# Kernel tuning notes

Measured on AMD Instinct MI355X. Metric: run time of the kernel, lower is better.

Reference implementation:

```python
import jax, jax.numpy as jnp
import numpy as np

B, N0, NCLS = 8, 1024, 40
SPACING, SIGMA_FACTOR = 2.0, 1.0
BLOCKS = [[64, 64], [128, 128], [256, 1024]]
POOL_SIZES = [256, 64, 1]
FC1, FC2 = 512, 256
# 3x3x3 kernel translation grid (27-point support, hard-coded in ConvLayer)
GRID = jnp.asarray(np.array([[i, j, k] for i in (-1, 0, 1) for j in (-1, 0, 1) for k in (-1, 0, 1)], dtype=np.float32))  # [27,3]


def pcnn_conv(pc, feat, W, b, sigma):
    """Extension-operator point convolution.
    pc [B,N,3], feat [B,N,Cin], W [27,Cin,Cout], b [Cout].
    out[b,i,o] = relu( (1/N) * sum_l sum_j exp(-||p_i - p_j + t_l||^2/(2 ks^2)) f[b,j] @ W[l] + b )
    """
    ks = SIGMA_FACTOR * sigma
    trans = SPACING * sigma * GRID                      # [27,3]
    inv = 1.0 / (2.0 * ks * ks)
    diff = pc[:, :, None, :] - pc[:, None, :, :]        # [B,N,N,3]
    d2 = jnp.sum(diff * diff, -1)                       # [B,N,N]
    n = pc.shape[1]

    def body(acc, wt):
        t, Wl = wt                                      # t [3], Wl [Cin,Cout]
        # ||diff + t||^2 = d2 + 2 diff.t + |t|^2
        e = jnp.exp(-(d2 + 2.0 * jnp.einsum('bijd,d->bij', diff, t) + jnp.dot(t, t)) * inv)
        s = jnp.einsum('bij,bjc->bic', e, feat)         # Gaussian-weighted gather
        return acc + jnp.einsum('bic,co->bio', s, Wl), None

    out0 = jnp.zeros((pc.shape[0], n, W.shape[2]), feat.dtype)
    out, _ = jax.lax.scan(body, out0, (trans, W))
    return jax.nn.relu(out / n + b)


def fps(pts, m):
    """Farthest point sampling. pts [N,3] -> indices [m]."""
    d = jnp.sum((pts - pts[0]) ** 2, -1)
    idxs = jnp.zeros((m,), jnp.int32)

    def body(i, state):
        idxs, d = state
        nxt = jnp.argmax(d).astype(jnp.int32)
        idxs = idxs.at[i].set(nxt)
        d = jnp.minimum(d, jnp.sum((pts - pts[nxt]) ** 2, -1))
        return idxs, d

    idxs, _ = jax.lax.fori_loop(1, m, body, (idxs, d))
    return idxs


def pool(pc, feat, m):
    """FPS subsample to m centers, max-pool features over nearest-center clusters."""
    idx = jax.vmap(lambda p: fps(p, m))(pc)                      # [B,m]
    centers = jnp.take_along_axis(pc, idx[..., None], axis=1)    # [B,m,3]
    dist = jnp.sum((pc[:, :, None, :] - centers[:, None, :, :]) ** 2, -1)  # [B,N,m]
    assign = jnp.argmin(dist, -1)                                # [B,N]
    pooled = jax.vmap(lambda f, a: jax.ops.segment_max(f, a, num_segments=m))(feat, assign)
    return centers, pooled


def bn(x, g, b):
    mu = jnp.mean(x, 0)
    v = jnp.var(x, 0)
    return g * (x - mu) * jax.lax.rsqrt(v + 1e-5) + b


def setup_inputs() -> dict:
    key = jax.random.key(0)
    ks = jax.random.split(key, 24)
    inp = {"pc": jax.random.normal(ks[0], (B, 3, N0), jnp.float32)}
    chans = [4, 64, 64, 128, 128, 256, 1024]
    for i, (ci, co) in enumerate(zip(chans[:-1], chans[1:])):
        inp[f"w_c{i}"] = jax.random.normal(ks[1 + i], (27, ci, co), jnp.float32) * 0.05
        inp[f"b_c{i}"] = jnp.zeros((co,), jnp.float32)
    inp["w_fc1"] = jax.random.normal(ks[10], (1024, FC1), jnp.float32) * 0.03
    inp["g_fc1"] = jnp.ones((FC1,), jnp.float32)
    inp["be_fc1"] = jnp.zeros((FC1,), jnp.float32)
    inp["w_fc2"] = jax.random.normal(ks[11], (FC1, FC2), jnp.float32) * 0.05
    inp["g_fc2"] = jnp.ones((FC2,), jnp.float32)
    inp["be_fc2"] = jnp.zeros((FC2,), jnp.float32)
    inp["w_fc3"] = jax.random.normal(ks[12], (FC2, NCLS), jnp.float32) * 0.05
    inp["b_fc3"] = jnp.zeros((NCLS,), jnp.float32)
    return inp


def reference(pc, w_c0, b_c0, w_c1, b_c1, w_c2, b_c2, w_c3, b_c3, w_c4, b_c4, w_c5, b_c5,
              w_fc1, g_fc1, be_fc1, w_fc2, g_fc2, be_fc2, w_fc3, b_fc3):
    pts = jnp.transpose(pc, (0, 2, 1))                           # [B,N,3]
    b_, n0, _ = pts.shape
    feat = jnp.concatenate([pts, jnp.ones((b_, n0, 1), pts.dtype)], -1)  # [B,N,4]
    sigma = 1.0 / float(np.sqrt(n0))  # faithfully uses initial N for all blocks
    ws = [(w_c0, b_c0), (w_c1, b_c1), (w_c2, b_c2), (w_c3, b_c3), (w_c4, b_c4), (w_c5, b_c5)]
    idx = 0
    cur = pts
    for bi, block in enumerate(BLOCKS):
        for _ in block:
            W, bb = ws[idx]
            feat = pcnn_conv(cur, feat, W, bb, sigma)
            idx += 1
        cur, feat = pool(cur, feat, POOL_SIZES[bi])
    x = feat.reshape(b_, -1)                                     # [B,1024]
    x = jax.nn.relu(bn(x @ w_fc1, g_fc1, be_fc1))
    x = jax.nn.relu(bn(x @ w_fc2, g_fc2, be_fc2))
    return x @ w_fc3 + b_fc3
```

## Files before the change

kernel.cpp:

```cpp
#include <hip/hip_runtime.h>
#include <cstdint>
#include <cstddef>
#include <cmath>

constexpr int B = 8;
constexpr int N0 = 1024;
constexpr int CAP = 64;
using u16 = unsigned short;

typedef __bf16 bf16x8 __attribute__((ext_vector_type(8)));
typedef float f32x4 __attribute__((ext_vector_type(4)));

__device__ inline u16 f2bf(float x) {
  unsigned u = __float_as_uint(x);
  return (u16)((u + 0x7fffu + ((u >> 16) & 1u)) >> 16);
}
__device__ inline float bf2f(u16 h) { return __uint_as_float(((unsigned)h) << 16); }
__device__ inline int swk2(int row, int k) {
  int s = (((row >> 2) ^ (row >> 4)) & 3);
  return ((((k >> 3) ^ s) << 3) | (k & 7));
}

__global__ __launch_bounds__(256) void k_prep(const float* __restrict__ pc,
                                              float* __restrict__ pts,
                                              float* __restrict__ feat0,
                                              uint4* __restrict__ p3, int n3,
                                              uint4* __restrict__ p6, int n6,
                                              uint4* __restrict__ p9, int n9) {
  int idx = blockIdx.x * blockDim.x + threadIdx.x;
  if (idx < B * N0) {
    int b = idx / N0, i = idx - b * N0;
    float x = pc[(b * 3 + 0) * N0 + i];
    float y = pc[(b * 3 + 1) * N0 + i];
    float z = pc[(b * 3 + 2) * N0 + i];
    pts[idx * 3 + 0] = x; pts[idx * 3 + 1] = y; pts[idx * 3 + 2] = z;
    feat0[idx * 4 + 0] = x; feat0[idx * 4 + 1] = y; feat0[idx * 4 + 2] = z; feat0[idx * 4 + 3] = 1.0f;
  }
  uint4 v = make_uint4(0xFFFFFFFFu, 0xFFFFFFFFu, 0xFFFFFFFFu, 0xFFFFFFFFu);
  for (int i = idx; i < n3; i += B * N0) p3[i] = v;
  for (int i = idx; i < n6; i += B * N0) p6[i] = v;
  for (int i = idx; i < n9; i += B * N0) p9[i] = v;
}

__global__ __launch_bounds__(256) void k_pairs(const float* __restrict__ pts,
                                               int* __restrict__ pidx, int* __restrict__ pcnt,
                                               int N) {
  const int r = blockIdx.x * 4 + (threadIdx.x >> 6);
  const int lane = threadIdx.x & 63;
  const int b = r / N;
  const float px = pts[(size_t)r * 3 + 0];
  const float py = pts[(size_t)r * 3 + 1];
  const float pz = pts[(size_t)r * 3 + 2];
  int* row = pidx + (size_t)r * CAP;
  int base = 0;
  for (int j0 = 0; j0 < N; j0 += 64) {
    int j = j0 + lane;
    float dx = px - pts[((size_t)b * N + j) * 3 + 0];
    float dy = py - pts[((size_t)b * N + j) * 3 + 1];
    float dz = pz - pts[((size_t)b * N + j) * 3 + 2];
    float d2 = dx * dx + dy * dy + dz * dz;
    bool keep = d2 <= 0.1228f;
    unsigned long long mk = __ballot(keep);
    int pos = __popcll(mk & ((1ull << lane) - 1ull));
    if (keep) { int s = base + pos; if (s < CAP) row[s] = j; }
    base += __popcll(mk);
  }
  if (lane == 0) pcnt[r] = base < CAP ? base : CAP;
}

__global__ void k_econtract(const float* __restrict__ pts, const float* __restrict__ feat,
                            const int* __restrict__ pidx, const int* __restrict__ pcnt,
                            u16* __restrict__ Shi, u16* __restrict__ Slo,
                            int N, int Cin, int K, int Kpad, int mbase) {
  const int g = mbase + blockIdx.x;
  const int b = g / N;
  const int t = threadIdx.x;
  const bool cact = t < Cin;
  const float px = pts[(size_t)g * 3 + 0];
  const float py = pts[(size_t)g * 3 + 1];
  const float pz = pts[(size_t)g * 3 + 2];
  float acc[27];
#pragma unroll
  for (int l = 0; l < 27; ++l) acc[l] = 0.f;
  const int n = pcnt[g];
  const int* row = pidx + (size_t)g * CAP;
  for (int p = 0; p < n; ++p) {
    int j = row[p];
    size_t jb = (size_t)b * N + j;
    float dx = px - pts[jb * 3 + 0];
    float dy = py - pts[jb * 3 + 1];
    float dz = pz - pts[jb * 3 + 2];
    float d2 = dx * dx + dy * dy + dz * dz;
    float base_ = __expf(-512.f * d2);
    float gxv[3] = {__expf(64.f * dx - 2.f), 1.f, __expf(-64.f * dx - 2.f)};
    float gyv[3] = {__expf(64.f * dy - 2.f), 1.f, __expf(-64.f * dy - 2.f)};
    float gzv[3] = {__expf(64.f * dz - 2.f), 1.f, __expf(-64.f * dz - 2.f)};
    float fv = cact ? feat[jb * Cin + t] : 0.f;
#pragma unroll
    for (int a = 0; a < 3; ++a) {
      float ba = base_ * gxv[a];
#pragma unroll
      for (int b2 = 0; b2 < 3; ++b2) {
        float bab = ba * gyv[b2];
#pragma unroll
        for (int c2 = 0; c2 < 3; ++c2) {
          int l = a * 9 + b2 * 3 + c2;
          acc[l] = fmaf(bab * gzv[c2], fv, acc[l]);
        }
      }
    }
  }
  size_t rowo = (size_t)blockIdx.x * Kpad;
  if (cact) {
#pragma unroll
    for (int l = 0; l < 27; ++l) {
      float v = acc[l];
      u16 h = f2bf(v);
      u16 lo = f2bf(v - bf2f(h));
      Shi[rowo + (size_t)l * Cin + t] = h;
      Slo[rowo + (size_t)l * Cin + t] = lo;
    }
  }
  if (Kpad > K && t >= Cin && t < Cin + (Kpad - K)) {
    size_t po = rowo + K + (t - Cin);
    Shi[po] = 0; Slo[po] = 0;
  }
}

__global__ __launch_bounds__(512) void k_gemm_mfma(const u16* __restrict__ Shi,
                                                   const u16* __restrict__ Slo,
                                                   const float* __restrict__ W,
                                                   const float* __restrict__ bias,
                                                   float* __restrict__ out,
                                                   float* __restrict__ P,
                                                   int K, int Kpad, int Cout, float scale,
                                                   int mcur) {
  __shared__ u16 As[2][2][32][40];
  __shared__ u16 Bs[2][2][64][40];
  __shared__ float xch[4][64][8];
  const int t = threadIdx.x;
  const int h = t >> 8;
  const int tl = t & 255;
  const int nb = blockIdx.x * 64;
  const int m0 = blockIdx.y * 32;
  const int l = t & 63, w = t >> 6;
  const int ks = w >> 2, wq = w & 3;
  const int wm = (wq >> 1) * 16, wn = (wq & 1) * 32;
  const int la = l & 15, lg = l >> 4;
  const int ntiles = Kpad >> 6;
  const int KZ = gridDim.z, z = blockIdx.z;
  const int q = ntiles / KZ, r = ntiles % KZ;
  const int t0 = z * q + (z < r ? z : r);
  const int cnt = q + (z < r ? 1 : 0);
  const int ar = tl >> 3, ak = (tl & 7) * 4;
  const size_t aOff = (size_t)(m0 + ar) * Kpad + h * 32 + ak;
  const int aw = swk2(ar, ak);
  const int kp = (tl >> 4) * 2, n4 = (tl & 15) * 4;
  f32x4 acc0 = {0.f, 0.f, 0.f, 0.f}, acc1 = {0.f, 0.f, 0.f, 0.f};

  for (int kt = 0; kt < cnt; ++kt) {
    const int k0 = (t0 + kt) * 64;
    *(ushort4*)&As[h][0][ar][aw] = *(const ushort4*)(Shi + aOff + k0);
    *(ushort4*)&As[h][1][ar][aw] = *(const ushort4*)(Slo + aOff + k0);
    {
      int gk0 = k0 + h * 32 + kp;
      float4 b0 = make_float4(0.f, 0.f, 0.f, 0.f), b1 = b0;
      if (gk0 < K) b0 = *(const float4*)(W + (size_t)gk0 * Cout + nb + n4);
      if (gk0 + 1 < K) b1 = *(const float4*)(W + (size_t)(gk0 + 1) * Cout + nb + n4);
      float v0[4] = {b0.x, b0.y, b0.z, b0.w};
      float v1[4] = {b1.x, b1.y, b1.z, b1.w};
#pragma unroll
      for (int e = 0; e < 4; ++e) {
        int n = n4 + e;
        int kw = swk2(n, kp);
        u16 h0 = f2bf(v0[e]);
        u16 l0 = f2bf(v0[e] - bf2f(h0));
        u16 h1 = f2bf(v1[e]);
        u16 l1 = f2bf(v1[e] - bf2f(h1));
        *(unsigned*)&Bs[h][0][n][kw] = (unsigned)h0 | ((unsigned)h1 << 16);
        *(unsigned*)&Bs[h][1][n][kw] = (unsigned)l0 | ((unsigned)l1 << 16);
      }
    }
    __syncthreads();
    bf16x8 ah = *(const bf16x8*)&As[ks][0][wm + la][swk2(wm + la, lg * 8)];
    bf16x8 al = *(const bf16x8*)&As[ks][1][wm + la][swk2(wm + la, lg * 8)];
    bf16x8 bh0 = *(const bf16x8*)&Bs[ks][0][wn + la][swk2(wn + la, lg * 8)];
    bf16x8 bl0 = *(const bf16x8*)&Bs[ks][1][wn + la][swk2(wn + la, lg * 8)];
    bf16x8 bh1 = *(const bf16x8*)&Bs[ks][0][wn + 16 + la][swk2(wn + 16 + la, lg * 8)];
    bf16x8 bl1 = *(const bf16x8*)&Bs[ks][1][wn + 16 + la][swk2(wn + 16 + la, lg * 8)];
    acc0 = __builtin_amdgcn_mfma_f32_16x16x32_bf16(ah, bh0, acc0, 0, 0, 0);
    acc1 = __builtin_amdgcn_mfma_f32_16x16x32_bf16(ah, bh1, acc1, 0, 0, 0);
    acc0 = __builtin_amdgcn_mfma_f32_16x16x32_bf16(al, bh0, acc0, 0, 0, 0);
    acc1 = __builtin_amdgcn_mfma_f32_16x16x32_bf16(al, bh1, acc1, 0, 0, 0);
    acc0 = __builtin_amdgcn_mfma_f32_16x16x32_bf16(ah, bl0, acc0, 0, 0, 0);
    acc1 = __builtin_amdgcn_mfma_f32_16x16x32_bf16(ah, bl1, acc1, 0, 0, 0);
    __syncthreads();
  }
  if (w >= 4) {
#pragma unroll
    for (int r2 = 0; r2 < 4; ++r2) { xch[wq][l][r2] = acc0[r2]; xch[wq][l][r2 + 4] = acc1[r2]; }
  }
  __syncthreads();
  if (w < 4) {
#pragma unroll
    for (int r2 = 0; r2 < 4; ++r2) { acc0[r2] += xch[wq][l][r2]; acc1[r2] += xch[wq][l][r2 + 4]; }
    if (gridDim.z == 1) {
#pragma unroll
      for (int r2 = 0; r2 < 4; ++r2) {
        int gm = m0 + wm + lg * 4 + r2;
        int gn0 = nb + wn + la;
        out[(size_t)gm * Cout + gn0] = fmaxf(fmaf(acc0[r2], scale, bias[gn0]), 0.f);
        int gn1 = gn0 + 16;
        out[(size_t)gm * Cout + gn1] = fmaxf(fmaf(acc1[r2], scale, bias[gn1]), 0.f);
      }
    } else {
      float* Pz = P + (size_t)z * mcur * Cout;
#pragma unroll
      for (int r2 = 0; r2 < 4; ++r2) {
        int gm = m0 + wm + lg * 4 + r2;
        int gn0 = nb + wn + la;
        Pz[(size_t)gm * Cout + gn0] = acc0[r2];
        Pz[(size_t)gm * Cout + gn0 + 16] = acc1[r2];
      }
    }
  }
}

__global__ __launch_bounds__(256) void k_reduce(const float* __restrict__ P,
                                                const float* __restrict__ bias,
                                                float* __restrict__ out,
                                                int n4, int Cout, int KZ, float scale,
                                                int stride) {
  int i = blockIdx.x * 256 + threadIdx.x;
  if (i >= n4) return;
  float4 s = *(const float4*)(P + (size_t)i * 4);
  for (int z = 1; z < KZ; ++z) {
    float4 v = *(const float4*)(P + (size_t)z * stride + (size_t)i * 4);
    s.x += v.x; s.y += v.y; s.z += v.z; s.w += v.w;
  }
  int c = (i * 4) % Cout;
  float4 bb = *(const float4*)(bias + c);
  float4 o;
  o.x = fmaxf(fmaf(s.x, scale, bb.x), 0.f);
  o.y = fmaxf(fmaf(s.y, scale, bb.y), 0.f);
  o.z = fmaxf(fmaf(s.z, scale, bb.z), 0.f);
  o.w = fmaxf(fmaf(s.w, scale, bb.w), 0.f);
  *(float4*)(out + (size_t)i * 4) = o;
}

template <int CTRL>
__device__ __forceinline__ float dppmaxf(float v) {
  int o = __builtin_amdgcn_update_dpp(0, __float_as_int(v), CTRL, 0xF, 0xF, true);
  return fmaxf(v, __int_as_float(o));
}
__device__ __forceinline__ float wavemaxf(float v) {
  v = dppmaxf<0xB1>(v);
  v = dppmaxf<0x4E>(v);
  v = dppmaxf<0x141>(v);
  v = dppmaxf<0x140>(v);
  v = dppmaxf<0x142>(v);
  v = dppmaxf<0x143>(v);
  return __uint_as_float((unsigned)__builtin_amdgcn_readlane(__float_as_int(v), 63));
}

#define FPS_LOAD(i) \
  float qx##i = src[3 * i + 0], qy##i = src[3 * i + 1], qz##i = src[3 * i + 2];
#define FPS_PIN(i) \
  asm volatile("" : "+v"(qx##i), "+v"(qy##i), "+v"(qz##i));
#define FPS_D0(i) \
  float d##i; { float ax = __fsub_rn(qx##i, x0), ay = __fsub_rn(qy##i, y0), az = __fsub_rn(qz##i, z0); \
    d##i = __fadd_rn(__fadd_rn(__fmul_rn(ax, ax), __fmul_rn(ay, ay)), __fmul_rn(az, az)); }
#define FPS_UPD(i) \
  { float ax = __fsub_rn(qx##i, cx), ay = __fsub_rn(qy##i, cy), az = __fsub_rn(qz##i, cz); \
    float nd = __fadd_rn(__fadd_rn(__fmul_rn(ax, ax), __fmul_rn(ay, ay)), __fmul_rn(az, az)); \
    d##i = fminf(d##i, nd); }
#define FPS_SEL(i) \
  { bool e = (d##i == lbest); sx = e ? qx##i : sx; sy = e ? qy##i : sy; sz = e ? qz##i : sz; }

__global__ __launch_bounds__(64, 1) void k_fps1024(const float* __restrict__ pts,
                                                   float* __restrict__ centers, int m) {
  const int b = blockIdx.x;
  const int t = threadIdx.x;
  const float* P = pts + (size_t)b * 1024 * 3;
  const float* src = P + t * 16 * 3;
  FPS_LOAD(0) FPS_LOAD(1) FPS_LOAD(2) FPS_LOAD(3)
  FPS_LOAD(4) FPS_LOAD(5) FPS_LOAD(6) FPS_LOAD(7)
  FPS_LOAD(8) FPS_LOAD(9) FPS_LOAD(10) FPS_LOAD(11)
  FPS_LOAD(12) FPS_LOAD(13) FPS_LOAD(14) FPS_LOAD(15)
  FPS_PIN(0) FPS_PIN(1) FPS_PIN(2) FPS_PIN(3)
  FPS_PIN(4) FPS_PIN(5) FPS_PIN(6) FPS_PIN(7)
  FPS_PIN(8) FPS_PIN(9) FPS_PIN(10) FPS_PIN(11)
  FPS_PIN(12) FPS_PIN(13) FPS_PIN(14) FPS_PIN(15)
  float x0 = P[0], y0 = P[1], z0 = P[2];
  FPS_D0(0) FPS_D0(1) FPS_D0(2) FPS_D0(3)
  FPS_D0(4) FPS_D0(5) FPS_D0(6) FPS_D0(7)
  FPS_D0(8) FPS_D0(9) FPS_D0(10) FPS_D0(11)
  FPS_D0(12) FPS_D0(13) FPS_D0(14) FPS_D0(15)
  if (t == 0) {
    centers[(size_t)b * m * 3 + 0] = x0;
    centers[(size_t)b * m * 3 + 1] = y0;
    centers[(size_t)b * m * 3 + 2] = z0;
  }
  for (int it = 1; it < m; ++it) {
    float lbest;
    {
      float a0 = fmaxf(d0, d1), a1 = fmaxf(d2, d3), a2 = fmaxf(d4, d5), a3 = fmaxf(d6, d7);
      float a4 = fmaxf(d8, d9), a5 = fmaxf(d10, d11), a6 = fmaxf(d12, d13), a7 = fmaxf(d14, d15);
      float b0 = fmaxf(a0, a1), b1 = fmaxf(a2, a3), b2 = fmaxf(a4, a5), b3 = fmaxf(a6, a7);
      lbest = fmaxf(fmaxf(b0, b1), fmaxf(b2, b3));
    }
    float sx = qx15, sy = qy15, sz = qz15;
    FPS_SEL(14) FPS_SEL(13) FPS_SEL(12) FPS_SEL(11)
    FPS_SEL(10) FPS_SEL(9) FPS_SEL(8) FPS_SEL(7)
    FPS_SEL(6) FPS_SEL(5) FPS_SEL(4) FPS_SEL(3)
    FPS_SEL(2) FPS_SEL(1) FPS_SEL(0)
    float wmax = wavemaxf(lbest);
    unsigned long long mask = __ballot(lbest == wmax);
    int fl = __ffsll((long long)mask) - 1;
    float cx = __uint_as_float((unsigned)__builtin_amdgcn_readlane(__float_as_int(sx), fl));
    float cy = __uint_as_float((unsigned)__builtin_amdgcn_readlane(__float_as_int(sy), fl));
    float cz = __uint_as_float((unsigned)__builtin_amdgcn_readlane(__float_as_int(sz), fl));
    if (t == 0) {
      centers[((size_t)b * m + it) * 3 + 0] = cx;
      centers[((size_t)b * m + it) * 3 + 1] = cy;
      centers[((size_t)b * m + it) * 3 + 2] = cz;
    }
    FPS_UPD(0) FPS_UPD(1) FPS_UPD(2) FPS_UPD(3)
    FPS_UPD(4) FPS_UPD(5) FPS_UPD(6) FPS_UPD(7)
    FPS_UPD(8) FPS_UPD(9) FPS_UPD(10) FPS_UPD(11)
    FPS_UPD(12) FPS_UPD(13) FPS_UPD(14) FPS_UPD(15)
  }
}

__global__ __launch_bounds__(64, 1) void k_fps256(const float* __restrict__ pts,
                                                  float* __restrict__ centers, int m) {
  const int b = blockIdx.x;
  const int t = threadIdx.x;
  const float* P = pts + (size_t)b * 256 * 3;
  const float* src = P + t * 4 * 3;
  FPS_LOAD(0) FPS_LOAD(1) FPS_LOAD(2) FPS_LOAD(3)
  FPS_PIN(0) FPS_PIN(1) FPS_PIN(2) FPS_PIN(3)
  float x0 = P[0], y0 = P[1], z0 = P[2];
  FPS_D0(0) FPS_D0(1) FPS_D0(2) FPS_D0(3)
  if (t == 0) {
    centers[(size_t)b * m * 3 + 0] = x0;
    centers[(size_t)b * m * 3 + 1] = y0;
    centers[(size_t)b * m * 3 + 2] = z0;
  }
  for (int it = 1; it < m; ++it) {
    float lbest = fmaxf(fmaxf(d0, d1), fmaxf(d2, d3));
    float sx = qx3, sy = qy3, sz = qz3;
    FPS_SEL(2) FPS_SEL(1) FPS_SEL(0)
    float wmax = wavemaxf(lbest);
    unsigned long long mask = __ballot(lbest == wmax);
    int fl = __ffsll((long long)mask) - 1;
    float cx = __uint_as_float((unsigned)__builtin_amdgcn_readlane(__float_as_int(sx), fl));
    float cy = __uint_as_float((unsigned)__builtin_amdgcn_readlane(__float_as_int(sy), fl));
    float cz = __uint_as_float((unsigned)__builtin_amdgcn_readlane(__float_as_int(sz), fl));
    if (t == 0) {
      centers[((size_t)b * m + it) * 3 + 0] = cx;
      centers[((size_t)b * m + it) * 3 + 1] = cy;
      centers[((size_t)b * m + it) * 3 + 2] = cz;
    }
    FPS_UPD(0) FPS_UPD(1) FPS_UPD(2) FPS_UPD(3)
  }
}

__global__ __launch_bounds__(64) void k_center0(const float* __restrict__ pts,
                                                float* __restrict__ centers,
                                                int* __restrict__ assign) {
  const int b = blockIdx.x, t = threadIdx.x;
  if (t < 3) centers[b * 3 + t] = pts[(size_t)b * 64 * 3 + t];
  assign[b * 64 + t] = 0;
}

__global__ __launch_bounds__(256) void k_assign(const float* __restrict__ pts,
                                                const float* __restrict__ centers,
                                                int* __restrict__ assign, int N, int m) {
  __shared__ float cs[256 * 3];
  const int t = threadIdx.x;
  const int idx = blockIdx.x * 256 + t;
  const int b = (blockIdx.x * 256) / N;
  for (int i = t; i < m * 3; i += 256) cs[i] = centers[(size_t)b * m * 3 + i];
  __syncthreads();
  float px = pts[(size_t)idx * 3 + 0], py = pts[(size_t)idx * 3 + 1], pz = pts[(size_t)idx * 3 + 2];
  float best = 3.4e38f; int bk = 0;
  for (int k = 0; k < m; ++k) {
    float dx = __fsub_rn(px, cs[k * 3 + 0]);
    float dy = __fsub_rn(py, cs[k * 3 + 1]);
    float dz = __fsub_rn(pz, cs[k * 3 + 2]);
    float dd = __fadd_rn(__fadd_rn(__fmul_rn(dx, dx), __fmul_rn(dy, dy)), __fmul_rn(dz, dz));
    if (dd < best) { best = dd; bk = k; }
  }
  assign[idx] = bk;
}

__global__ __launch_bounds__(256) void k_segmax(const float* __restrict__ feat,
                                                const int* __restrict__ assign,
                                                float* __restrict__ pooled,
                                                int N, int m, int C) {
  int idx = blockIdx.x * blockDim.x + threadIdx.x;
  if (idx >= B * N * C) return;
  int b = idx / (N * C);
  int r = idx - b * N * C;
  int i = r / C;
  int c = r - i * C;
  int a = assign[b * N + i];
  atomicMax((int*)&pooled[((size_t)b * m + a) * C + c], __float_as_int(feat[idx]));
}

template <int K, int COUT, bool BNR>
__global__ __launch_bounds__(256) void k_fc(const float* __restrict__ x,
                                            const float* __restrict__ w,
                                            const float* __restrict__ g,
                                            const float* __restrict__ be,
                                            float* __restrict__ out) {
  __shared__ float ys[8][33];
  int t = threadIdx.x;
  int n = t >> 5, cl = t & 31;
  int c = blockIdx.x * 32 + cl;
  float acc = 0.f;
  if (c < COUT) {
    const float* xr = x + n * K;
    float a0 = 0.f, a1 = 0.f, a2 = 0.f, a3 = 0.f;
    for (int k = 0; k < K; k += 4) {
      a0 = fmaf(xr[k + 0], w[(size_t)(k + 0) * COUT + c], a0);
      a1 = fmaf(xr[k + 1], w[(size_t)(k + 1) * COUT + c], a1);
      a2 = fmaf(xr[k + 2], w[(size_t)(k + 2) * COUT + c], a2);
      a3 = fmaf(xr[k + 3], w[(size_t)(k + 3) * COUT + c], a3);
    }
    acc = (a0 + a1) + (a2 + a3);
  }
  ys[n][cl] = acc;
  __syncthreads();
  if (c >= COUT) return;
  if (BNR) {
    float mu = 0.f;
#pragma unroll
    for (int q = 0; q < 8; ++q) mu += ys[q][cl];
    mu *= 0.125f;
    float var = 0.f;
#pragma unroll
    for (int q = 0; q < 8; ++q) { float dv = ys[q][cl] - mu; var = fmaf(dv, dv, var); }
    var *= 0.125f;
    float rs = 1.f / sqrtf(var + 1e-5f);
    float v = g[c] * (acc - mu) * rs + be[c];
    out[n * COUT + c] = fmaxf(v, 0.f);
  } else {
    out[n * COUT + c] = acc + be[c];
  }
}

extern "C" void kernel_launch(void* const* d_in, const int* in_sizes, int n_in,
                              void* d_out, int out_size, void* d_ws, size_t ws_size,
                              hipStream_t stream) {
  (void)in_sizes; (void)n_in; (void)out_size;
  const float* pc = (const float*)d_in[0];
  const float* Wc[6]; const float* bc[6];
  for (int l = 0; l < 6; ++l) { Wc[l] = (const float*)d_in[1 + 2 * l]; bc[l] = (const float*)d_in[2 + 2 * l]; }
  const float* w1 = (const float*)d_in[13];
  const float* g1 = (const float*)d_in[14];
  const float* be1 = (const float*)d_in[15];
  const float* w2 = (const float*)d_in[16];
  const float* g2 = (const float*)d_in[17];
  const float* be2 = (const float*)d_in[18];
  const float* w3 = (const float*)d_in[19];
  const float* b3 = (const float*)d_in[20];

  float* ws = (float*)d_ws;
  size_t o = 0;
  auto A = [&](size_t n) { size_t r = o; o += (n + 63) & ~(size_t)63; return r; };
  const size_t PTS0 = A((size_t)B * 1024 * 3);
  const size_t PTS1 = A((size_t)B * 256 * 3);
  const size_t PTS2 = A((size_t)B * 64 * 3);
  const size_t PTS3 = A((size_t)B * 3);
  const size_t F0  = A((size_t)B * 1024 * 4);
  const size_t FB1 = A((size_t)B * 1024 * 64);
  const size_t FB2 = A((size_t)B * 1024 * 64);
  const size_t FB3 = A((size_t)B * 256 * 64);
  const size_t FB4 = A((size_t)B * 256 * 128);
  const size_t FB5 = A((size_t)B * 256 * 128);
  const size_t FB6 = A((size_t)B * 64 * 128);
  const size_t FB7 = A((size_t)B * 64 * 256);
  const size_t FB8 = A((size_t)B * 64 * 1024);
  const size_t FB9 = A((size_t)B * 1024);
  const size_t ASSIGN = A((size_t)B * 1024);
  const size_t Y1 = A((size_t)8 * 512);
  const size_t Y2 = A((size_t)8 * 256);
  const size_t PIDX = A((size_t)B * 1024 * CAP);
  const size_t PCNT = A((size_t)B * 1024);
  const size_t dynB = o * sizeof(float);

  int* pidx = (int*)(ws + PIDX);
  int* pcnt = (int*)(ws + PCNT);

  k_prep<<<dim3((B * N0 + 255) / 256), dim3(256), 0, stream>>>(
      pc, ws + PTS0, ws + F0,
      (uint4*)(ws + FB3), B * 256 * 64 / 4,
      (uint4*)(ws + FB6), B * 64 * 128 / 4,
      (uint4*)(ws + FB9), B * 1024 / 4);

  auto conv = [&](size_t ptsOff, size_t finOff, size_t foutOff, int Npts, int Cin, int Cout,
                  const float* W, const float* bias) {
    const int M = B * Npts;
    const int K = 27 * Cin;
    const int Kpad = (K + 63) & ~63;
    const size_t availB = (ws_size > dynB) ? ws_size - dynB : 0;
    size_t pResB = availB / 4;
    if (pResB > (size_t)13 << 20) pResB = (size_t)13 << 20;
    const size_t sByte = availB - pResB;
    long mc = (long)(sByte / ((size_t)Kpad * 4)) & ~31L;
    int Mc = (int)((mc < (long)M) ? mc : (long)M);
    if (Mc < 32) Mc = 32;
    u16* Shi = (u16*)((char*)d_ws + dynB);
    u16* Slo = Shi + (size_t)Mc * Kpad;
    float* P = (float*)(Shi + (size_t)2 * Mc * Kpad);
    const int mch = (M + Mc - 1) / Mc;
    const float scale = 1.f / (float)Npts;
    const int blk = (Cin <= 64) ? 64 : Cin;
    const int ntiles = Kpad >> 6;
    for (int mcb = 0; mcb < mch; ++mcb) {
      const int mb0 = mcb * Mc;
      const int mcur = ((M - mb0) < Mc) ? (M - mb0) : Mc;
      k_econtract<<<dim3(mcur), dim3(blk), 0, stream>>>(ws + ptsOff, ws + finOff, pidx, pcnt,
                                                        Shi, Slo, Npts, Cin, K, Kpad, mb0);
      const int gx = Cout / 64, gy = mcur / 32;
      int kz = 1024 / (gx * gy);
      if (kz < 1) kz = 1;
      if (kz > ntiles) kz = ntiles;
      if (kz > 16) kz = 16;
      long pcap = (long)(pResB / ((size_t)mcur * Cout * 4));
      if ((long)kz > pcap) kz = (pcap < 1) ? 1 : (int)pcap;
      float* outp = ws + foutOff + (size_t)mb0 * Cout;
      k_gemm_mfma<<<dim3(gx, gy, kz), dim3(512), 0, stream>>>(
          Shi, Slo, W, bias, outp, P, K, Kpad, Cout, scale, mcur);
      if (kz > 1) {
        int n4 = mcur * Cout / 4;
        k_reduce<<<dim3((n4 + 255) / 256), dim3(256), 0, stream>>>(
            P, bias, outp, n4, Cout, kz, scale, mcur * Cout);
      }
    }
  };

  k_pairs<<<dim3(B * 1024 / 4), dim3(256), 0, stream>>>(ws + PTS0, pidx, pcnt, 1024);
  conv(PTS0, F0, FB1, 1024, 4, 64, Wc[0], bc[0]);
  conv(PTS0, FB1, FB2, 1024, 64, 64, Wc[1], bc[1]);
  k_fps1024<<<dim3(B), dim3(64), 0, stream>>>(ws + PTS0, ws + PTS1, 256);
  k_assign<<<dim3(B * 1024 / 256), dim3(256), 0, stream>>>(ws + PTS0, ws + PTS1, (int*)(ws + ASSIGN), 1024, 256);
  k_segmax<<<dim3((B * 1024 * 64 + 255) / 256), dim3(256), 0, stream>>>(ws + FB2, (int*)(ws + ASSIGN), ws + FB3, 1024, 256, 64);
  k_pairs<<<dim3(B * 256 / 4), dim3(256), 0, stream>>>(ws + PTS1, pidx, pcnt, 256);
  conv(PTS1, FB3, FB4, 256, 64, 128, Wc[2], bc[2]);
  conv(PTS1, FB4, FB5, 256, 128, 128, Wc[3], bc[3]);
  k_fps256<<<dim3(B), dim3(64), 0, stream>>>(ws + PTS1, ws + PTS2, 64);
  k_assign<<<dim3(B * 256 / 256), dim3(256), 0, stream>>>(ws + PTS1, ws + PTS2, (int*)(ws + ASSIGN), 256, 64);
  k_segmax<<<dim3((B * 256 * 128 + 255) / 256), dim3(256), 0, stream>>>(ws + FB5, (int*)(ws + ASSIGN), ws + FB6, 256, 64, 128);
  k_pairs<<<dim3(B * 64 / 4), dim3(256), 0, stream>>>(ws + PTS2, pidx, pcnt, 64);
  conv(PTS2, FB6, FB7, 64, 128, 256, Wc[4], bc[4]);
  conv(PTS2, FB7, FB8, 64, 256, 1024, Wc[5], bc[5]);
  k_center0<<<dim3(B), dim3(64), 0, stream>>>(ws + PTS2, ws + PTS3, (int*)(ws + ASSIGN));
  k_segmax<<<dim3((B * 64 * 1024 + 255) / 256), dim3(256), 0, stream>>>(ws + FB8, (int*)(ws + ASSIGN), ws + FB9, 64, 1, 1024);
  k_fc<1024, 512, true><<<dim3(512 / 32), dim3(256), 0, stream>>>(ws + FB9, w1, g1, be1, ws + Y1);
  k_fc<512, 256, true><<<dim3(256 / 32), dim3(256), 0, stream>>>(ws + Y1, w2, g2, be2, ws + Y2);
  k_fc<256, 40, false><<<dim3(2), dim3(256), 0, stream>>>(ws + Y2, w3, nullptr, b3, (float*)d_out);
}
```

Baseline: 434.0 us.

## Fuse FPS into econtract launch and compute 27 Gaussian weights per lane

Farthest point sampling no longer runs as its own serial launch. It now occupies B extra blocks appended to the econtract grid of the preceding conv, so its long single-wave loop overlaps with the econtract work instead of sitting between kernels. Separately, econtract now has lanes 0-26 each compute one of the 27 translated Gaussian weights with a single exp, share them through LDS, and let every channel thread read them. This replaces the per-thread 7 exps and product tree. The cost is an LDS round-trip with an explicit waitcnt on every neighbor iteration, plus launch_bounds(64,1) on the fused kernel, which may limit econtract occupancy.

After: 426.9 us. About the same (-1.6%).

```diff
diff --git a/kernel.cpp b/kernel.cpp
--- a/kernel.cpp
+++ b/kernel.cpp
@@ -68,17 +68,30 @@
   if (lane == 0) pcnt[r] = base < CAP ? base : CAP;
 }
 
-__global__ void k_econtract(const float* __restrict__ pts, const float* __restrict__ feat,
-                            const int* __restrict__ pidx, const int* __restrict__ pcnt,
-                            u16* __restrict__ Shi, u16* __restrict__ Slo,
-                            int N, int Cin, int K, int Kpad, int mbase) {
-  const int g = mbase + blockIdx.x;
+__device__ __forceinline__ void econ_dev(float (*eL)[28],
+                                         const float* __restrict__ pts,
+                                         const float* __restrict__ feat,
+                                         const int* __restrict__ pidx,
+                                         const int* __restrict__ pcnt,
+                                         u16* __restrict__ Shi, u16* __restrict__ Slo,
+                                         int N, int Cin, int K, int Kpad, int mbase,
+                                         int blockX) {
+  const int g = mbase + blockX;
   const int b = g / N;
   const int t = threadIdx.x;
+  const int w = t >> 6, lane = t & 63;
   const bool cact = t < Cin;
   const float px = pts[(size_t)g * 3 + 0];
   const float py = pts[(size_t)g * 3 + 1];
   const float pz = pts[(size_t)g * 3 + 2];
+  float sxc = 0.f, syc = 0.f, szc = 0.f, cst = 0.f;
+  if (lane < 27) {
+    int a = lane / 9, bb = (lane / 3) % 3, cc = lane % 3;
+    sxc = (a == 0) ? 64.f : ((a == 2) ? -64.f : 0.f);
+    syc = (bb == 0) ? 64.f : ((bb == 2) ? -64.f : 0.f);
+    szc = (cc == 0) ? 64.f : ((cc == 2) ? -64.f : 0.f);
+    cst = -2.f * (float)((a != 1) + (bb != 1) + (cc != 1));
+  }
   float acc[27];
 #pragma unroll
   for (int l = 0; l < 27; ++l) acc[l] = 0.f;
@@ -91,26 +104,17 @@
     float dy = py - pts[jb * 3 + 1];
     float dz = pz - pts[jb * 3 + 2];
     float d2 = dx * dx + dy * dy + dz * dz;
-    float base_ = __expf(-512.f * d2);
-    float gxv[3] = {__expf(64.f * dx - 2.f), 1.f, __expf(-64.f * dx - 2.f)};
-    float gyv[3] = {__expf(64.f * dy - 2.f), 1.f, __expf(-64.f * dy - 2.f)};
-    float gzv[3] = {__expf(64.f * dz - 2.f), 1.f, __expf(-64.f * dz - 2.f)};
+    if (lane < 27) {
+      float ex = fmaf(-512.f, d2, fmaf(sxc, dx, fmaf(syc, dy, fmaf(szc, dz, cst))));
+      eL[w][lane] = __expf(ex);
+    }
+    asm volatile("s_waitcnt lgkmcnt(0)" ::: "memory");
+    __builtin_amdgcn_sched_barrier(0);
     float fv = cact ? feat[jb * Cin + t] : 0.f;
 #pragma unroll
-    for (int a = 0; a < 3; ++a) {
-      float ba = base_ * gxv[a];
-#pragma unroll
-      for (int b2 = 0; b2 < 3; ++b2) {
-        float bab = ba * gyv[b2];
-#pragma unroll
-        for (int c2 = 0; c2 < 3; ++c2) {
-          int l = a * 9 + b2 * 3 + c2;
-          acc[l] = fmaf(bab * gzv[c2], fv, acc[l]);
-        }
-      }
-    }
-  }
-  size_t rowo = (size_t)blockIdx.x * Kpad;
+    for (int l = 0; l < 27; ++l) acc[l] = fmaf(eL[w][l], fv, acc[l]);
+  }
+  size_t rowo = (size_t)blockX * Kpad;
   if (cact) {
 #pragma unroll
     for (int l = 0; l < 27; ++l) {
@@ -125,6 +129,144 @@
     size_t po = rowo + K + (t - Cin);
     Shi[po] = 0; Slo[po] = 0;
   }
+}
+
+__global__ void k_econtract(const float* __restrict__ pts, const float* __restrict__ feat,
+                            const int* __restrict__ pidx, const int* __restrict__ pcnt,
+                            u16* __restrict__ Shi, u16* __restrict__ Slo,
+                            int N, int Cin, int K, int Kpad, int mbase) {
+  __shared__ float eL[4][28];
+  econ_dev(eL, pts, feat, pidx, pcnt, Shi, Slo, N, Cin, K, Kpad, mbase, blockIdx.x);
+}
+
+template <int CTRL>
+__device__ __forceinline__ float dppmaxf(float v) {
+  int o = __builtin_amdgcn_update_dpp(0, __float_as_int(v), CTRL, 0xF, 0xF, true);
+  return fmaxf(v, __int_as_float(o));
+}
+__device__ __forceinline__ float wavemaxf(float v) {
+  v = dppmaxf<0xB1>(v);
+  v = dppmaxf<0x4E>(v);
+  v = dppmaxf<0x141>(v);
+  v = dppmaxf<0x140>(v);
+  v = dppmaxf<0x142>(v);
+  v = dppmaxf<0x143>(v);
+  return __uint_as_float((unsigned)__builtin_amdgcn_readlane(__float_as_int(v), 63));
+}
+
+#define FPS_LOAD(i) \
+  float qx##i = src[3 * i + 0], qy##i = src[3 * i + 1], qz##i = src[3 * i + 2];
+#define FPS_PIN(i) \
+  asm volatile("" : "+v"(qx##i), "+v"(qy##i), "+v"(qz##i));
+#define FPS_D0(i) \
+  float d##i; { float ax = __fsub_rn(qx##i, x0), ay = __fsub_rn(qy##i, y0), az = __fsub_rn(qz##i, z0); \
+    d##i = __fadd_rn(__fadd_rn(__fmul_rn(ax, ax), __fmul_rn(ay, ay)), __fmul_rn(az, az)); }
+#define FPS_UPD(i) \
+  { float ax = __fsub_rn(qx##i, cx), ay = __fsub_rn(qy##i, cy), az = __fsub_rn(qz##i, cz); \
+    float nd = __fadd_rn(__fadd_rn(__fmul_rn(ax, ax), __fmul_rn(ay, ay)), __fmul_rn(az, az)); \
+    d##i = fminf(d##i, nd); }
+#define FPS_SEL(i) \
+  { bool e = (d##i == lbest); sx = e ? qx##i : sx; sy = e ? qy##i : sy; sz = e ? qz##i : sz; }
+
+__device__ __noinline__ void fps1024_dev(const float* __restrict__ P,
+                                         float* __restrict__ centers, int m, int b, int t) {
+  const float* src = P + t * 16 * 3;
+  FPS_LOAD(0) FPS_LOAD(1) FPS_LOAD(2) FPS_LOAD(3)
+  FPS_LOAD(4) FPS_LOAD(5) FPS_LOAD(6) FPS_LOAD(7)
+  FPS_LOAD(8) FPS_LOAD(9) FPS_LOAD(10) FPS_LOAD(11)
+  FPS_LOAD(12) FPS_LOAD(13) FPS_LOAD(14) FPS_LOAD(15)
+  FPS_PIN(0) FPS_PIN(1) FPS_PIN(2) FPS_PIN(3)
+  FPS_PIN(4) FPS_PIN(5) FPS_PIN(6) FPS_PIN(7)
+  FPS_PIN(8) FPS_PIN(9) FPS_PIN(10) FPS_PIN(11)
+  FPS_PIN(12) FPS_PIN(13) FPS_PIN(14) FPS_PIN(15)
+  float x0 = P[0], y0 = P[1], z0 = P[2];
+  FPS_D0(0) FPS_D0(1) FPS_D0(2) FPS_D0(3)
+  FPS_D0(4) FPS_D0(5) FPS_D0(6) FPS_D0(7)
+  FPS_D0(8) FPS_D0(9) FPS_D0(10) FPS_D0(11)
+  FPS_D0(12) FPS_D0(13) FPS_D0(14) FPS_D0(15)
+  if (t == 0) {
+    centers[(size_t)b * m * 3 + 0] = x0;
+    centers[(size_t)b * m * 3 + 1] = y0;
+    centers[(size_t)b * m * 3 + 2] = z0;
+  }
+  for (int it = 1; it < m; ++it) {
+    float lbest;
+    {
+      float a0 = fmaxf(d0, d1), a1 = fmaxf(d2, d3), a2 = fmaxf(d4, d5), a3 = fmaxf(d6, d7);
+      float a4 = fmaxf(d8, d9), a5 = fmaxf(d10, d11), a6 = fmaxf(d12, d13), a7 = fmaxf(d14, d15);
+      float b0 = fmaxf(a0, a1), b1 = fmaxf(a2, a3), b2 = fmaxf(a4, a5), b3 = fmaxf(a6, a7);
+      lbest = fmaxf(fmaxf(b0, b1), fmaxf(b2, b3));
+    }
+    float sx = qx15, sy = qy15, sz = qz15;
+    FPS_SEL(14) FPS_SEL(13) FPS_SEL(12) FPS_SEL(11)
+    FPS_SEL(10) FPS_SEL(9) FPS_SEL(8) FPS_SEL(7)
+    FPS_SEL(6) FPS_SEL(5) FPS_SEL(4) FPS_SEL(3)
+    FPS_SEL(2) FPS_SEL(1) FPS_SEL(0)
+    float wmax = wavemaxf(lbest);
+    unsigned long long mask = __ballot(lbest == wmax);
+    int fl = __ffsll((long long)mask) - 1;
+    float cx = __uint_as_float((unsigned)__builtin_amdgcn_readlane(__float_as_int(sx), fl));
+    float cy = __uint_as_float((unsigned)__builtin_amdgcn_readlane(__float_as_int(sy), fl));
+    float cz = __uint_as_float((unsigned)__builtin_amdgcn_readlane(__float_as_int(sz), fl));
+    if (t == 0) {
+      centers[((size_t)b * m + it) * 3 + 0] = cx;
+      centers[((size_t)b * m + it) * 3 + 1] = cy;
+      centers[((size_t)b * m + it) * 3 + 2] = cz;
+    }
+    FPS_UPD(0) FPS_UPD(1) FPS_UPD(2) FPS_UPD(3)
+    FPS_UPD(4) FPS_UPD(5) FPS_UPD(6) FPS_UPD(7)
+    FPS_UPD(8) FPS_UPD(9) FPS_UPD(10) FPS_UPD(11)
+    FPS_UPD(12) FPS_UPD(13) FPS_UPD(14) FPS_UPD(15)
+  }
+}
+
+__device__ __noinline__ void fps256_dev(const float* __restrict__ P,
+                                        float* __restrict__ centers, int m, int b, int t) {
+  const float* src = P + t * 4 * 3;
+  FPS_LOAD(0) FPS_LOAD(1) FPS_LOAD(2) FPS_LOAD(3)
+  FPS_PIN(0) FPS_PIN(1) FPS_PIN(2) FPS_PIN(3)
+  float x0 = P[0], y0 = P[1], z0 = P[2];
+  FPS_D0(0) FPS_D0(1) FPS_D0(2) FPS_D0(3)
+  if (t == 0) {
+    centers[(size_t)b * m * 3 + 0] = x0;
+    centers[(size_t)b * m * 3 + 1] = y0;
+    centers[(size_t)b * m * 3 + 2] = z0;
+  }
+  for (int it = 1; it < m; ++it) {
+    float lbest = fmaxf(fmaxf(d0, d1), fmaxf(d2, d3));
+    float sx = qx3, sy = qy3, sz = qz3;
+    FPS_SEL(2) FPS_SEL(1) FPS_SEL(0)
+    float wmax = wavemaxf(lbest);
+    unsigned long long mask = __ballot(lbest == wmax);
+    int fl = __ffsll((long long)mask) - 1;
+    float cx = __uint_as_float((unsigned)__builtin_amdgcn_readlane(__float_as_int(sx), fl));
+    float cy = __uint_as_float((unsigned)__builtin_amdgcn_readlane(__float_as_int(sy), fl));
+    float cz = __uint_as_float((unsigned)__builtin_amdgcn_readlane(__float_as_int(sz), fl));
+    if (t == 0) {
+      centers[((size_t)b * m + it) * 3 + 0] = cx;
+      centers[((size_t)b * m + it) * 3 + 1] = cy;
+      centers[((size_t)b * m + it) * 3 + 2] = cz;
+    }
+    FPS_UPD(0) FPS_UPD(1) FPS_UPD(2) FPS_UPD(3)
+  }
+}
+
+__global__ __launch_bounds__(64, 1) void k_econtract_fps(
+    const float* __restrict__ pts, const float* __restrict__ feat,
+    const int* __restrict__ pidx, const int* __restrict__ pcnt,
+    u16* __restrict__ Shi, u16* __restrict__ Slo,
+    int N, int Cin, int K, int Kpad, int mbase,
+    int fpsMode, const float* __restrict__ fpsPts, float* __restrict__ fpsCenters, int fpsM) {
+  __shared__ float eL[4][28];
+  const int nEcon = gridDim.x - B;
+  if ((int)blockIdx.x >= nEcon) {
+    const int b = blockIdx.x - nEcon;
+    const int t = threadIdx.x;
+    if (fpsMode == 1) fps1024_dev(fpsPts + (size_t)b * 1024 * 3, fpsCenters, fpsM, b, t);
+    else fps256_dev(fpsPts + (size_t)b * 256 * 3, fpsCenters, fpsM, b, t);
+    return;
+  }
+  econ_dev(eL, pts, feat, pidx, pcnt, Shi, Slo, N, Cin, K, Kpad, mbase, blockIdx.x);
 }
 
 __global__ __launch_bounds__(512) void k_gemm_mfma(const u16* __restrict__ Shi,
@@ -248,124 +390,6 @@
   *(float4*)(out + (size_t)i * 4) = o;
 }
 
-template <int CTRL>
-__device__ __forceinline__ float dppmaxf(float v) {
-  int o = __builtin_amdgcn_update_dpp(0, __float_as_int(v), CTRL, 0xF, 0xF, true);
-  return fmaxf(v, __int_as_float(o));
-}
-__device__ __forceinline__ float wavemaxf(float v) {
-  v = dppmaxf<0xB1>(v);
-  v = dppmaxf<0x4E>(v);
-  v = dppmaxf<0x141>(v);
-  v = dppmaxf<0x140>(v);
-  v = dppmaxf<0x142>(v);
-  v = dppmaxf<0x143>(v);
-  return __uint_as_float((unsigned)__builtin_amdgcn_readlane(__float_as_int(v), 63));
-}
-
-#define FPS_LOAD(i) \
-  float qx##i = src[3 * i + 0], qy##i = src[3 * i + 1], qz##i = src[3 * i + 2];
-#define FPS_PIN(i) \
-  asm volatile("" : "+v"(qx##i), "+v"(qy##i), "+v"(qz##i));
-#define FPS_D0(i) \
-  float d##i; { float ax = __fsub_rn(qx##i, x0), ay = __fsub_rn(qy##i, y0), az = __fsub_rn(qz##i, z0); \
-    d##i = __fadd_rn(__fadd_rn(__fmul_rn(ax, ax), __fmul_rn(ay, ay)), __fmul_rn(az, az)); }
-#define FPS_UPD(i) \
-  { float ax = __fsub_rn(qx##i, cx), ay = __fsub_rn(qy##i, cy), az = __fsub_rn(qz##i, cz); \
-    float nd = __fadd_rn(__fadd_rn(__fmul_rn(ax, ax), __fmul_rn(ay, ay)), __fmul_rn(az, az)); \
-    d##i = fminf(d##i, nd); }
-#define FPS_SEL(i) \
-  { bool e = (d##i == lbest); sx = e ? qx##i : sx; sy = e ? qy##i : sy; sz = e ? qz##i : sz; }
-
-__global__ __launch_bounds__(64, 1) void k_fps1024(const float* __restrict__ pts,
-                                                   float* __restrict__ centers, int m) {
-  const int b = blockIdx.x;
-  const int t = threadIdx.x;
-  const float* P = pts + (size_t)b * 1024 * 3;
-  const float* src = P + t * 16 * 3;
-  FPS_LOAD(0) FPS_LOAD(1) FPS_LOAD(2) FPS_LOAD(3)
-  FPS_LOAD(4) FPS_LOAD(5) FPS_LOAD(6) FPS_LOAD(7)
-  FPS_LOAD(8) FPS_LOAD(9) FPS_LOAD(10) FPS_LOAD(11)
-  FPS_LOAD(12) FPS_LOAD(13) FPS_LOAD(14) FPS_LOAD(15)
-  FPS_PIN(0) FPS_PIN(1) FPS_PIN(2) FPS_PIN(3)
-  FPS_PIN(4) FPS_PIN(5) FPS_PIN(6) FPS_PIN(7)
-  FPS_PIN(8) FPS_PIN(9) FPS_PIN(10) FPS_PIN(11)
-  FPS_PIN(12) FPS_PIN(13) FPS_PIN(14) FPS_PIN(15)
-  float x0 = P[0], y0 = P[1], z0 = P[2];
-  FPS_D0(0) FPS_D0(1) FPS_D0(2) FPS_D0(3)
-  FPS_D0(4) FPS_D0(5) FPS_D0(6) FPS_D0(7)
-  FPS_D0(8) FPS_D0(9) FPS_D0(10) FPS_D0(11)
-  FPS_D0(12) FPS_D0(13) FPS_D0(14) FPS_D0(15)
-  if (t == 0) {
-    centers[(size_t)b * m * 3 + 0] = x0;
-    centers[(size_t)b * m * 3 + 1] = y0;
-    centers[(size_t)b * m * 3 + 2] = z0;
-  }
-  for (int it = 1; it < m; ++it) {
-    float lbest;
-    {
-      float a0 = fmaxf(d0, d1), a1 = fmaxf(d2, d3), a2 = fmaxf(d4, d5), a3 = fmaxf(d6, d7);
-      float a4 = fmaxf(d8, d9), a5 = fmaxf(d10, d11), a6 = fmaxf(d12, d13), a7 = fmaxf(d14, d15);
-      float b0 = fmaxf(a0, a1), b1 = fmaxf(a2, a3), b2 = fmaxf(a4, a5), b3 = fmaxf(a6, a7);
-      lbest = fmaxf(fmaxf(b0, b1), fmaxf(b2, b3));
-    }
-    float sx = qx15, sy = qy15, sz = qz15;
-    FPS_SEL(14) FPS_SEL(13) FPS_SEL(12) FPS_SEL(11)
-    FPS_SEL(10) FPS_SEL(9) FPS_SEL(8) FPS_SEL(7)
-    FPS_SEL(6) FPS_SEL(5) FPS_SEL(4) FPS_SEL(3)
-    FPS_SEL(2) FPS_SEL(1) FPS_SEL(0)
-    float wmax = wavemaxf(lbest);
-    unsigned long long mask = __ballot(lbest == wmax);
-    int fl = __ffsll((long long)mask) - 1;
-    float cx = __uint_as_float((unsigned)__builtin_amdgcn_readlane(__float_as_int(sx), fl));
-    float cy = __uint_as_float((unsigned)__builtin_amdgcn_readlane(__float_as_int(sy), fl));
-    float cz = __uint_as_float((unsigned)__builtin_amdgcn_readlane(__float_as_int(sz), fl));
-    if (t == 0) {
-      centers[((size_t)b * m + it) * 3 + 0] = cx;
-      centers[((size_t)b * m + it) * 3 + 1] = cy;
-      centers[((size_t)b * m + it) * 3 + 2] = cz;
-    }
-    FPS_UPD(0) FPS_UPD(1) FPS_UPD(2) FPS_UPD(3)
-    FPS_UPD(4) FPS_UPD(5) FPS_UPD(6) FPS_UPD(7)
-    FPS_UPD(8) FPS_UPD(9) FPS_UPD(10) FPS_UPD(11)
-    FPS_UPD(12) FPS_UPD(13) FPS_UPD(14) FPS_UPD(15)
-  }
-}
-
-__global__ __launch_bounds__(64, 1) void k_fps256(const float* __restrict__ pts,
-                                                  float* __restrict__ centers, int m) {
-  const int b = blockIdx.x;
-  const int t = threadIdx.x;
-  const float* P = pts + (size_t)b * 256 * 3;
-  const float* src = P + t * 4 * 3;
-  FPS_LOAD(0) FPS_LOAD(1) FPS_LOAD(2) FPS_LOAD(3)
-  FPS_PIN(0) FPS_PIN(1) FPS_PIN(2) FPS_PIN(3)
-  float x0 = P[0], y0 = P[1], z0 = P[2];
-  FPS_D0(0) FPS_D0(1) FPS_D0(2) FPS_D0(3)
-  if (t == 0) {
-    centers[(size_t)b * m * 3 + 0] = x0;
-    centers[(size_t)b * m * 3 + 1] = y0;
-    centers[(size_t)b * m * 3 + 2] = z0;
-  }
-  for (int it = 1; it < m; ++it) {
-    float lbest = fmaxf(fmaxf(d0, d1), fmaxf(d2, d3));
-    float sx = qx3, sy = qy3, sz = qz3;
-    FPS_SEL(2) FPS_SEL(1) FPS_SEL(0)
-    float wmax = wavemaxf(lbest);
-    unsigned long long mask = __ballot(lbest == wmax);
-    int fl = __ffsll((long long)mask) - 1;
-    float cx = __uint_as_float((unsigned)__builtin_amdgcn_readlane(__float_as_int(sx), fl));
-    float cy = __uint_as_float((unsigned)__builtin_amdgcn_readlane(__float_as_int(sy), fl));
-    float cz = __uint_as_float((unsigned)__builtin_amdgcn_readlane(__float_as_int(sz), fl));
-    if (t == 0) {
-      centers[((size_t)b * m + it) * 3 + 0] = cx;
-      centers[((size_t)b * m + it) * 3 + 1] = cy;
-      centers[((size_t)b * m + it) * 3 + 2] = cz;
-    }
-    FPS_UPD(0) FPS_UPD(1) FPS_UPD(2) FPS_UPD(3)
-  }
-}
-
 __global__ __launch_bounds__(64) void k_center0(const float* __restrict__ pts,
                                                 float* __restrict__ centers,
                                                 int* __restrict__ assign) {
@@ -501,7 +525,8 @@
       (uint4*)(ws + FB9), B * 1024 / 4);
 
   auto conv = [&](size_t ptsOff, size_t finOff, size_t foutOff, int Npts, int Cin, int Cout,
-                  const float* W, const float* bias) {
+                  const float* W, const float* bias,
+                  int fpsMode, size_t fpsPtsOff, size_t fpsCtrOff, int fpsM) {
     const int M = B * Npts;
     const int K = 27 * Cin;
     const int Kpad = (K + 63) & ~63;
@@ -522,8 +547,14 @@
     for (int mcb = 0; mcb < mch; ++mcb) {
       const int mb0 = mcb * Mc;
       const int mcur = ((M - mb0) < Mc) ? (M - mb0) : Mc;
-      k_econtract<<<dim3(mcur), dim3(blk), 0, stream>>>(ws + ptsOff, ws + finOff, pidx, pcnt,
-                                                        Shi, Slo, Npts, Cin, K, Kpad, mb0);
+      if (mcb == 0 && fpsMode && blk == 64) {
+        k_econtract_fps<<<dim3(mcur + B), dim3(64), 0, stream>>>(
+            ws + ptsOff, ws + finOff, pidx, pcnt, Shi, Slo, Npts, Cin, K, Kpad, mb0,
+            fpsMode, ws + fpsPtsOff, ws + fpsCtrOff, fpsM);
+      } else {
+        k_econtract<<<dim3(mcur), dim3(blk), 0, stream>>>(ws + ptsOff, ws + finOff, pidx, pcnt,
+                                                          Shi, Slo, Npts, Cin, K, Kpad, mb0);
+      }
       const int gx = Cout / 64, gy = mcur / 32;
       int kz = 1024 / (gx * gy);
       if (kz < 1) kz = 1;
@@ -543,20 +574,18 @@
   };
 
   k_pairs<<<dim3(B * 1024 / 4), dim3(256), 0, stream>>>(ws + PTS0, pidx, pcnt, 1024);
-  conv(PTS0, F0, FB1, 1024, 4, 64, Wc[0], bc[0]);
-  conv(PTS0, FB1, FB2, 1024, 64, 64, Wc[1], bc[1]);
-  k_fps1024<<<dim3(B), dim3(64), 0, stream>>>(ws + PTS0, ws + PTS1, 256);
+  conv(PTS0, F0, FB1, 1024, 4, 64, Wc[0], bc[0], 0, 0, 0, 0);
+  conv(PTS0, FB1, FB2, 1024, 64, 64, Wc[1], bc[1], 1, PTS0, PTS1, 256);
   k_assign<<<dim3(B * 1024 / 256), dim3(256), 0, stream>>>(ws + PTS0, ws + PTS1, (int*)(ws + ASSIGN), 1024, 256);
   k_segmax<<<dim3((B * 1024 * 64 + 255) / 256), dim3(256), 0, stream>>>(ws + FB2, (int*)(ws + ASSIGN), ws + FB3, 1024, 256, 64);
   k_pairs<<<dim3(B * 256 / 4), dim3(256), 0, stream>>>(ws + PTS1, pidx, pcnt, 256);
-  conv(PTS1, FB3, FB4, 256, 64, 128, Wc[2], bc[2]);
-  conv(PTS1, FB4, FB5, 256, 128, 128, Wc[3], bc[3]);
-  k_fps256<<<dim3(B), dim3(64), 0, stream>>>(ws + PTS1, ws + PTS2, 64);
+  conv(PTS1, FB3, FB4, 256, 64, 128, Wc[2], bc[2], 2, PTS1, PTS2, 64);
+  conv(PTS1, FB4, FB5, 256, 128, 128, Wc[3], bc[3], 0, 0, 0, 0);
   k_assign<<<dim3(B * 256 / 256), dim3(256), 0, stream>>>(ws + PTS1, ws + PTS2, (int*)(ws + ASSIGN), 256, 64);
   k_segmax<<<dim3((B * 256 * 128 + 255) / 256), dim3(256), 0, stream>>>(ws + FB5, (int*)(ws + ASSIGN), ws + FB6, 256, 64, 128);
   k_pairs<<<dim3(B * 64 / 4), dim3(256), 0, stream>>>(ws + PTS2, pidx, pcnt, 64);
-  conv(PTS2, FB6, FB7, 64, 128, 256, Wc[4], bc[4]);
-  conv(PTS2, FB7, FB8, 64, 256, 1024, Wc[5], bc[5]);
+  conv(PTS2, FB6, FB7, 64, 128, 256, Wc[4], bc[4], 0, 0, 0, 0);
+  conv(PTS2, FB7, FB8, 64, 256, 1024, Wc[5], bc[5], 0, 0, 0, 0);
   k_center0<<<dim3(B), dim3(64), 0, stream>>>(ws + PTS2, ws + PTS3, (int*)(ws + ASSIGN));
   k_segmax<<<dim3((B * 64 * 1024 + 255) / 256), dim3(256), 0, stream>>>(ws + FB8, (int*)(ws + ASSIGN), ws + FB9, 64, 1, 1024);
   k_fc<1024, 512, true><<<dim3(512 / 32), dim3(256), 0, stream>>>(ws + FB9, w1, g1, be1, ws + Y1);
```
